# Kernel tuning notes

Measured on AMD Instinct MI355X. Metric: run time of the kernel, lower is better.

Reference implementation:

```python
import jax, jax.numpy as jnp
import numpy as np

B, S, D = 4, 2048, 256
H, RANK, DFF = 8, 8, 1024
DK = D // H
EPS = 1e-5


def _linear(x, W, b):
    # torch nn.Linear: y = x @ W.T + b, W shape (out, in)
    return jnp.einsum('bsd,od->bso', x, W) + b


def _layer_norm(x, g, b):
    mu = jnp.mean(x, axis=-1, keepdims=True)
    var = jnp.var(x, axis=-1, keepdims=True)
    return (x - mu) * jax.lax.rsqrt(var + EPS) * g + b


def setup_inputs() -> dict:
    key = jax.random.key(0)
    ks = jax.random.split(key, 20)
    r = RANK * H
    s = lambda fan_in: 1.0 / np.sqrt(fan_in)
    inp = {
        'x': jax.random.normal(ks[0], (B, S, D), jnp.float32),
        'Wq_down': jax.random.uniform(ks[1], (r, D), jnp.float32, -s(D), s(D)),
        'bq_down': jnp.zeros((r,), jnp.float32),
        'Wq_up': jax.random.uniform(ks[2], (D, r), jnp.float32, -s(r), s(r)),
        'bq_up': jnp.zeros((D,), jnp.float32),
        'Wk_down': jax.random.uniform(ks[3], (r, D), jnp.float32, -s(D), s(D)),
        'bk_down': jnp.zeros((r,), jnp.float32),
        'Wk_up': jax.random.uniform(ks[4], (D, r), jnp.float32, -s(r), s(r)),
        'bk_up': jnp.zeros((D,), jnp.float32),
        'Wv': jax.random.uniform(ks[5], (D, D), jnp.float32, -s(D), s(D)),
        'bv': jnp.zeros((D,), jnp.float32),
        'Wo': jax.random.uniform(ks[6], (D, D), jnp.float32, -s(D), s(D)),
        'bo': jnp.zeros((D,), jnp.float32),
        'ln_attn_g': jnp.ones((D,), jnp.float32),
        'ln_attn_b': jnp.zeros((D,), jnp.float32),
        'W_ff1': jax.random.uniform(ks[7], (DFF, D), jnp.float32, -s(D), s(D)),
        'b_ff1': jnp.zeros((DFF,), jnp.float32),
        'W_ff2': jax.random.uniform(ks[8], (D, DFF), jnp.float32, -s(DFF), s(DFF)),
        'b_ff2': jnp.zeros((D,), jnp.float32),
        'ln_blk_g': jnp.ones((D,), jnp.float32),
        'ln_blk_b': jnp.zeros((D,), jnp.float32),
    }
    return inp


def reference(x, Wq_down, bq_down, Wq_up, bq_up, Wk_down, bk_down, Wk_up, bk_up,
              Wv, bv, Wo, bo, ln_attn_g, ln_attn_b,
              W_ff1, b_ff1, W_ff2, b_ff2, ln_blk_g, ln_blk_b):
    # Low-rank Q/K: down-project to rank*H then up-project to D
    Q = _linear(_linear(x, Wq_down, bq_down), Wq_up, bq_up)
    K = _linear(_linear(x, Wk_down, bk_down), Wk_up, bk_up)
    V = _linear(x, Wv, bv)
    # (B,S,D) -> (B,H,S,DK)
    Q = Q.reshape(B, S, H, DK).transpose(0, 2, 1, 3)
    K = K.reshape(B, S, H, DK).transpose(0, 2, 1, 3)
    V = V.reshape(B, S, H, DK).transpose(0, 2, 1, 3)
    scale = 1.0 / np.sqrt(DK).astype(np.float32)
    scores = jnp.einsum('bhqd,bhkd->bhqk', Q, K) * scale
    attn = jax.nn.softmax(scores, axis=-1)
    context = jnp.einsum('bhqk,bhkd->bhqd', attn, V)
    context = context.transpose(0, 2, 1, 3).reshape(B, S, D)
    attn_out = _linear(context, Wo, bo)
    attn_out = _layer_norm(x + attn_out, ln_attn_g, ln_attn_b)
    # FFN: Linear -> GELU (exact erf, torch default) -> Linear
    h = jax.nn.gelu(_linear(attn_out, W_ff1, b_ff1), approximate=False)
    ff = _linear(h, W_ff2, b_ff2)
    return _layer_norm(attn_out + ff, ln_blk_g, ln_blk_b)
```

## Files before the change

### kernel.cpp

```cpp
#include <hip/hip_runtime.h>
#include <hip/hip_bf16.h>
#include <math.h>

#define NB 4
#define NS 2048
#define ND 256
#define NH 8
#define NDK 32
#define NDFF 1024
#define NROWS (NB * NS)
#define KC 2
#define KVB 64
#define KTILES (NS / KC / KVB)

using short8 = __attribute__((ext_vector_type(8))) short;
using f32x4  = __attribute__((ext_vector_type(4))) float;

__device__ __forceinline__ unsigned short f2bf(float f) {
  union { float f; unsigned u; } v; v.f = f;
  unsigned r = v.u + 0x7fffu + ((v.u >> 16) & 1u);
  return (unsigned short)(r >> 16);
}
__device__ __forceinline__ float bf2f(unsigned short u) {
  union { unsigned u; float f; } v; v.u = ((unsigned)u) << 16;
  return v.f;
}
__device__ __forceinline__ unsigned cvt_pk_bf16(float lo, float hi) {
  unsigned r;
  asm("v_cvt_pk_bf16_f32 %0, %1, %2" : "=v"(r) : "v"(lo), "v"(hi));
  return r;
}
__device__ __forceinline__ void gl_lds16(const void* g, void* l) {
  __builtin_amdgcn_global_load_lds(
      (const __attribute__((address_space(1))) unsigned int*)g,
      (__attribute__((address_space(3))) unsigned int*)l, 16, 0, 0);
}

__global__ void cvt_batch(const float* s0, const float* s1, const float* s2,
                          const float* s3, const float* s4, const float* s5,
                          const float* s6, const float* s7, const float* s8,
                          unsigned short* d0, unsigned short* d1,
                          unsigned short* d2, unsigned short* d3,
                          unsigned short* d4, unsigned short* d5,
                          unsigned short* d6, unsigned short* d7,
                          unsigned short* d8,
                          int n0, int n1, int n2, int n3, int n4, int n5,
                          int n6, int n7, int n8) {
  const float* s; unsigned short* d; int n;
  switch (blockIdx.y) {
    case 0: s = s0; d = d0; n = n0; break;
    case 1: s = s1; d = d1; n = n1; break;
    case 2: s = s2; d = d2; n = n2; break;
    case 3: s = s3; d = d3; n = n3; break;
    case 4: s = s4; d = d4; n = n4; break;
    case 5: s = s5; d = d5; n = n5; break;
    case 6: s = s6; d = d6; n = n6; break;
    case 7: s = s7; d = d7; n = n7; break;
    default: s = s8; d = d8; n = n8; break;
  }
  for (int i = (blockIdx.x * 256 + threadIdx.x) * 4; i < n; i += 512 * 256 * 4) {
    float4 v = *reinterpret_cast<const float4*>(s + i);
    ushort4 o;
    o.x = f2bf(v.x); o.y = f2bf(v.y); o.z = f2bf(v.z); o.w = f2bf(v.w);
    *reinterpret_cast<ushort4*>(d + i) = o;
  }
}

template <int BM, int ACT, int OBF, int RES>
__global__ __launch_bounds__(256)
void gemm_nt(const unsigned short* __restrict__ A, int lda,
             const unsigned short* __restrict__ W,
             const float* __restrict__ bias, const float* __restrict__ bias2,
             int bsplit, const float* __restrict__ resid,
             void* __restrict__ outp, int K, int O) {
  constexpr int MFW = BM / 32;
  __shared__ __align__(16) unsigned short lA[2][BM * 64];
  __shared__ __align__(16) unsigned short lB[2][64 * 64];
  const int tid = threadIdx.x, lane = tid & 63, wid = tid >> 6;
  const int wr = wid >> 1, wc = wid & 1;
  const int l15 = lane & 15, lg = lane >> 4;
  const int bm = blockIdx.x, bn = blockIdx.y;

  auto stage = [&](int k0, int buf) {
#pragma unroll
    for (int it = 0; it < BM / 32; ++it) {
      int c = it * 256 + tid;
      int row = c >> 3, cc = (c & 7) ^ (row & 7);
      gl_lds16(A + (size_t)(bm * BM + row) * lda + k0 + cc * 8,
               &lA[buf][c * 8]);
    }
#pragma unroll
    for (int it = 0; it < 2; ++it) {
      int c = it * 256 + tid;
      int row = c >> 3, cc = (c & 7) ^ (row & 7);
      gl_lds16(W + (size_t)(bn * 64 + row) * K + k0 + cc * 8, &lB[buf][c * 8]);
    }
  };

  f32x4 acc[MFW][2];
#pragma unroll
  for (int i = 0; i < MFW; ++i)
#pragma unroll
    for (int j = 0; j < 2; ++j) acc[i][j] = (f32x4)0.0f;

  const int T = K >> 6;
  stage(0, 0);
  __syncthreads();
  for (int t = 0; t < T; ++t) {
    const int cur = t & 1;
    if (t + 1 < T) stage((t + 1) << 6, cur ^ 1);
#pragma unroll
    for (int kk = 0; kk < 2; ++kk) {
      short8 a[MFW], b[2];
#pragma unroll
      for (int mf = 0; mf < MFW; ++mf) {
        int row = wr * (BM / 2) + mf * 16 + l15;
        a[mf] = *reinterpret_cast<const short8*>(
            &lA[cur][row * 64 + (((kk * 4 + lg) ^ (l15 & 7)) << 3)]);
      }
#pragma unroll
      for (int nf = 0; nf < 2; ++nf) {
        int row = wc * 32 + nf * 16 + l15;
        b[nf] = *reinterpret_cast<const short8*>(
            &lB[cur][row * 64 + (((kk * 4 + lg) ^ (l15 & 7)) << 3)]);
      }
#pragma unroll
      for (int mf = 0; mf < MFW; ++mf)
#pragma unroll
        for (int nf = 0; nf < 2; ++nf)
          acc[mf][nf] = __builtin_amdgcn_mfma_f32_16x16x32_bf16(
              a[mf], b[nf], acc[mf][nf], 0, 0, 0);
    }
    __syncthreads();
  }

#pragma unroll
  for (int mf = 0; mf < MFW; ++mf)
#pragma unroll
    for (int nf = 0; nf < 2; ++nf) {
      int col = bn * 64 + wc * 32 + nf * 16 + l15;
      float bv = (bias2 && col >= bsplit) ? bias2[col - bsplit] : bias[col];
#pragma unroll
      for (int i = 0; i < 4; ++i) {
        int row = bm * BM + wr * (BM / 2) + mf * 16 + lg * 4 + i;
        float v = acc[mf][nf][i] + bv;
        if (ACT == 1) v = 0.5f * v * (1.0f + erff(v * 0.70710678118654752f));
        if (RES) v += resid[(size_t)row * O + col];
        if (OBF)
          ((unsigned short*)outp)[(size_t)row * O + col] = f2bf(v);
        else
          ((float*)outp)[(size_t)row * O + col] = v;
      }
    }
}

__global__ __launch_bounds__(256)
void attn_kernel(const unsigned short* __restrict__ Qb,
                 const unsigned short* __restrict__ Kb,
                 const unsigned short* __restrict__ Vb,
                 unsigned short* __restrict__ pacc,
                 float* __restrict__ pl) {
  __shared__ __align__(16) unsigned short lK[2][KVB * 32];
  __shared__ __align__(16) unsigned short lVt[2][32 * 72];
  __shared__ __align__(16) unsigned short lP[4][16 * 64];
  const int tid = threadIdx.x, lane = tid & 63, wid = tid >> 6;
  const int l15 = lane & 15, lg = lane >> 4;
  const int qt = blockIdx.x, bh = blockIdx.y, kc = blockIdx.z;
  const int b = bh >> 3, h = bh & 7;
  const size_t headoff = (size_t)h * NDK;
  const int qbase = qt * 128 + wid * 32;
  const int kv0 = kc * (NS / KC);
  const float qscale = 0.25508686f;

  short8 aq[2];
#pragma unroll
  for (int r = 0; r < 2; ++r) {
    short8 v = *reinterpret_cast<const short8*>(
        Qb + (size_t)(b * NS + qbase + r * 16 + l15) * ND + headoff + lg * 8);
#pragma unroll
    for (int j = 0; j < 8; ++j)
      v[j] = (short)f2bf(bf2f((unsigned short)v[j]) * qscale);
    aq[r] = v;
  }

  const unsigned short* kptr =
      Kb + (size_t)(b * NS + kv0 + (tid >> 2)) * ND + headoff + (tid & 3) * 8;
  const int vd0 = (tid & 15) * 2, vk0 = (tid >> 4) * 4;
  const unsigned short* vptr =
      Vb + (size_t)(b * NS + kv0 + vk0) * ND + headoff + vd0;
  const size_t kvstride = (size_t)KVB * ND;

  auto writeV = [&](const unsigned* w, int buf) {
    unsigned lo0 = (w[0] & 0xffffu) | (w[1] << 16);
    unsigned lo1 = (w[2] & 0xffffu) | (w[3] << 16);
    unsigned hi0 = (w[0] >> 16) | (w[1] & 0xffff0000u);
    unsigned hi1 = (w[2] >> 16) | (w[3] & 0xffff0000u);
    *reinterpret_cast<uint2*>(&lVt[buf][vd0 * 72 + vk0]) = make_uint2(lo0, lo1);
    *reinterpret_cast<uint2*>(&lVt[buf][(vd0 + 1) * 72 + vk0]) =
        make_uint2(hi0, hi1);
  };

  f32x4 accT[2][2];
#pragma unroll
  for (int r = 0; r < 2; ++r)
#pragma unroll
    for (int d = 0; d < 2; ++d) accT[r][d] = (f32x4)0.0f;
  float l[2] = {0.0f, 0.0f};

  unsigned vr[4];
  gl_lds16(kptr, &lK[0][tid * 8]);
#pragma unroll
  for (int u = 0; u < 4; ++u)
    vr[u] = *reinterpret_cast<const unsigned*>(vptr + (size_t)u * ND);
  writeV(vr, 0);
  __syncthreads();

  for (int kt = 0; kt < KTILES; ++kt) {
    const int cur = kt & 1, nxt = cur ^ 1;
    const bool pf = (kt + 1 < KTILES);
    if (pf) {
      kptr += kvstride;
      vptr += kvstride;
      gl_lds16(kptr, &lK[nxt][tid * 8]);
#pragma unroll
      for (int u = 0; u < 4; ++u)
        vr[u] = *reinterpret_cast<const unsigned*>(vptr + (size_t)u * ND);
    }

#pragma unroll
    for (int r = 0; r < 2; ++r) {
      f32x4 sT[4];
      __builtin_amdgcn_s_setprio(1);
#pragma unroll
      for (int t = 0; t < 4; ++t) {
        short8 bk = *reinterpret_cast<const short8*>(
            &lK[cur][(t * 16 + l15) * 32 + lg * 8]);
        sT[t] = __builtin_amdgcn_mfma_f32_16x16x32_bf16(
            bk, aq[r], (f32x4)0.0f, 0, 0, 0);
      }
      __builtin_amdgcn_s_setprio(0);
#pragma unroll
      for (int t = 0; t < 4; ++t) {
        float p0 = __builtin_amdgcn_exp2f(sT[t][0]);
        float p1 = __builtin_amdgcn_exp2f(sT[t][1]);
        float p2 = __builtin_amdgcn_exp2f(sT[t][2]);
        float p3 = __builtin_amdgcn_exp2f(sT[t][3]);
        l[r] += (p0 + p1) + (p2 + p3);
        unsigned w0 = cvt_pk_bf16(p0, p1);
        unsigned w1 = cvt_pk_bf16(p2, p3);
        int blk = (t << 1) | (lg >> 1);
        *reinterpret_cast<uint2*>(
            &lP[wid][l15 * 64 + ((blk ^ (l15 & 7)) << 3) + ((lg & 1) << 2)]) =
            make_uint2(w0, w1);
      }
      __builtin_amdgcn_s_setprio(1);
#pragma unroll
      for (int kk = 0; kk < 2; ++kk) {
        short8 pa = *reinterpret_cast<const short8*>(
            &lP[wid][l15 * 64 + (((kk * 4 + lg) ^ (l15 & 7)) << 3)]);
#pragma unroll
        for (int dt = 0; dt < 2; ++dt) {
          short8 bv = *reinterpret_cast<const short8*>(
              &lVt[cur][(dt * 16 + l15) * 72 + kk * 32 + lg * 8]);
          accT[r][dt] = __builtin_amdgcn_mfma_f32_16x16x32_bf16(
              bv, pa, accT[r][dt], 0, 0, 0);
        }
      }
      __builtin_amdgcn_s_setprio(0);
    }

    if (pf) writeV(vr, nxt);
    __syncthreads();
  }

#pragma unroll
  for (int r = 0; r < 2; ++r) {
    l[r] += __shfl_xor(l[r], 16);
    l[r] += __shfl_xor(l[r], 32);
  }

#pragma unroll
  for (int r = 0; r < 2; ++r) {
    int qg = qbase + r * 16 + l15;
    size_t rowbase = ((size_t)kc * 65536 + (size_t)bh * NS + qg) * 32;
#pragma unroll
    for (int dt = 0; dt < 2; ++dt) {
      unsigned w0 = cvt_pk_bf16(accT[r][dt][0], accT[r][dt][1]);
      unsigned w1 = cvt_pk_bf16(accT[r][dt][2], accT[r][dt][3]);
      *reinterpret_cast<uint2*>(&pacc[rowbase + dt * 16 + lg * 4]) =
          make_uint2(w0, w1);
    }
  }
  if (lane < 16) {
#pragma unroll
    for (int r = 0; r < 2; ++r) {
      int qg = qbase + r * 16 + l15;
      pl[(size_t)kc * 65536 + (size_t)bh * NS + qg] = l[r];
    }
  }
}

__global__ __launch_bounds__(256)
void attn_combine(const unsigned short* __restrict__ pacc,
                  const float* __restrict__ pl,
                  unsigned short* __restrict__ ctx) {
  int gid = blockIdx.x * 256 + threadIdx.x;
  int r = gid >> 2, d8 = (gid & 3) * 8;
  float L = 0.0f;
#pragma unroll
  for (int c = 0; c < KC; ++c) L += pl[(size_t)c * 65536 + r];
  float inv = 1.0f / L;
  float o[8];
#pragma unroll
  for (int j = 0; j < 8; ++j) o[j] = 0.0f;
#pragma unroll
  for (int c = 0; c < KC; ++c) {
    short8 a = *reinterpret_cast<const short8*>(
        &pacc[((size_t)c * 65536 + r) * 32 + d8]);
#pragma unroll
    for (int j = 0; j < 8; ++j) o[j] += bf2f((unsigned short)a[j]);
  }
  int bh = r >> 11, q = r & 2047;
  int b = bh >> 3, h = bh & 7;
  short8 out;
#pragma unroll
  for (int j = 0; j < 8; ++j) out[j] = (short)f2bf(o[j] * inv);
  *reinterpret_cast<short8*>(
      &ctx[((size_t)(b * NS + q)) * ND + h * 32 + d8]) = out;
}

__global__ __launch_bounds__(256)
void ln_res_kernel(const float* __restrict__ a, const float* bsrc,
                   const float* __restrict__ g, const float* __restrict__ be,
                   float* yf, unsigned short* yb) {
  int row = blockIdx.x * 4 + (threadIdx.x >> 6);
  int lane = threadIdx.x & 63;
  size_t off = (size_t)row * ND + lane * 4;
  float4 va = *reinterpret_cast<const float4*>(a + off);
  float v0 = va.x, v1 = va.y, v2 = va.z, v3 = va.w;
  if (bsrc) {
    float4 vb = *reinterpret_cast<const float4*>(bsrc + off);
    v0 += vb.x; v1 += vb.y; v2 += vb.z; v3 += vb.w;
  }
  float s = v0 + v1 + v2 + v3;
  float sq = v0 * v0 + v1 * v1 + v2 * v2 + v3 * v3;
#pragma unroll
  for (int o = 1; o < 64; o <<= 1) {
    s += __shfl_xor(s, o);
    sq += __shfl_xor(sq, o);
  }
  float mu = s * (1.0f / 256.0f);
  float var = sq * (1.0f / 256.0f) - mu * mu;
  float rs = rsqrtf(var + 1e-5f);
  float4 vg = *reinterpret_cast<const float4*>(g + lane * 4);
  float4 vbe = *reinterpret_cast<const float4*>(be + lane * 4);
  float o0 = (v0 - mu) * rs * vg.x + vbe.x;
  float o1 = (v1 - mu) * rs * vg.y + vbe.y;
  float o2 = (v2 - mu) * rs * vg.z + vbe.z;
  float o3 = (v3 - mu) * rs * vg.w + vbe.w;
  if (yf) *reinterpret_cast<float4*>(yf + off) = make_float4(o0, o1, o2, o3);
  if (yb) {
    ushort4 ob;
    ob.x = f2bf(o0); ob.y = f2bf(o1); ob.z = f2bf(o2); ob.w = f2bf(o3);
    *reinterpret_cast<ushort4*>(yb + off) = ob;
  }
}

extern "C" void kernel_launch(void* const* d_in, const int* in_sizes, int n_in,
                              void* d_out, int out_size, void* d_ws,
                              size_t ws_size, hipStream_t stream) {
  (void)in_sizes; (void)n_in; (void)out_size; (void)ws_size;
  const float* x   = (const float*)d_in[0];
  const float* Wqd = (const float*)d_in[1];
  const float* bqd = (const float*)d_in[2];
  const float* Wqu = (const float*)d_in[3];
  const float* bqu = (const float*)d_in[4];
  const float* Wkd = (const float*)d_in[5];
  const float* bkd = (const float*)d_in[6];
  const float* Wku = (const float*)d_in[7];
  const float* bku = (const float*)d_in[8];
  const float* Wv  = (const float*)d_in[9];
  const float* bv  = (const float*)d_in[10];
  const float* Wo  = (const float*)d_in[11];
  const float* bo  = (const float*)d_in[12];
  const float* g1  = (const float*)d_in[13];
  const float* be1 = (const float*)d_in[14];
  const float* Wf1 = (const float*)d_in[15];
  const float* bf1 = (const float*)d_in[16];
  const float* Wf2 = (const float*)d_in[17];
  const float* bf2 = (const float*)d_in[18];
  const float* g2  = (const float*)d_in[19];
  const float* be2 = (const float*)d_in[20];

  char* p = (char*)d_ws;
  auto alloc = [&](size_t bytes) {
    char* r = p;
    p += (bytes + 255) & ~(size_t)255;
    return r;
  };
  unsigned short* xb   = (unsigned short*)alloc((size_t)NROWS * ND * 2);
  unsigned short* wqkd = (unsigned short*)alloc(128 * 256 * 2);
  unsigned short* wqu  = (unsigned short*)alloc(256 * 64 * 2);
  unsigned short* wku  = (unsigned short*)alloc(256 * 64 * 2);
  unsigned short* wv   = (unsigned short*)alloc(256 * 256 * 2);
  unsigned short* wo   = (unsigned short*)alloc(256 * 256 * 2);
  unsigned short* wf1  = (unsigned short*)alloc(1024 * 256 * 2);
  unsigned short* wf2  = (unsigned short*)alloc(256 * 1024 * 2);
  unsigned short* qkd  = (unsigned short*)alloc((size_t)NROWS * 128 * 2);
  unsigned short* Qb   = (unsigned short*)alloc((size_t)NROWS * ND * 2);
  unsigned short* Kb   = (unsigned short*)alloc((size_t)NROWS * ND * 2);
  unsigned short* Vb   = (unsigned short*)alloc((size_t)NROWS * ND * 2);
  unsigned short* ctx  = (unsigned short*)alloc((size_t)NROWS * ND * 2);
  float*          y1   = (float*)alloc((size_t)NROWS * ND * 4);
  unsigned short* y1b  = (unsigned short*)alloc((size_t)NROWS * ND * 2);
  unsigned short* hb   = (unsigned short*)alloc((size_t)NROWS * NDFF * 2);
  float* ao = (float*)d_out;

  unsigned short* pacc = hb;
  float* pl = y1;

  cvt_batch<<<dim3(512, 9), 256, 0, stream>>>(
      x, Wqd, Wkd, Wqu, Wku, Wv, Wo, Wf1, Wf2,
      xb, wqkd, wqkd + 64 * 256, wqu, wku, wv, wo, wf1, wf2,
      NROWS * ND, 64 * 256, 64 * 256, 256 * 64, 256 * 64, 256 * 256,
      256 * 256, 1024 * 256, 256 * 1024);

  gemm_nt<64, 0, 1, 0><<<dim3(128, 2), 256, 0, stream>>>(
      xb, 256, wqkd, bqd, bkd, 64, nullptr, qkd, 256, 128);
  gemm_nt<64, 0, 1, 0><<<dim3(128, 4), 256, 0, stream>>>(
      qkd, 128, wqu, bqu, nullptr, 0, nullptr, Qb, 64, 256);
  gemm_nt<64, 0, 1, 0><<<dim3(128, 4), 256, 0, stream>>>(
      qkd + 64, 128, wku, bku, nullptr, 0, nullptr, Kb, 64, 256);
  gemm_nt<64, 0, 1, 0><<<dim3(128, 4), 256, 0, stream>>>(
      xb, 256, wv, bv, nullptr, 0, nullptr, Vb, 256, 256);

  attn_kernel<<<dim3(NS / 128, NB * NH, KC), 256, 0, stream>>>(
      Qb, Kb, Vb, pacc, pl);
  attn_combine<<<dim3(1024), 256, 0, stream>>>(pacc, pl, ctx);

  gemm_nt<64, 0, 0, 1><<<dim3(128, 4), 256, 0, stream>>>(
      ctx, 256, wo, bo, nullptr, 0, x, ao, 256, 256);
  ln_res_kernel<<<NROWS / 4, 256, 0, stream>>>(ao, nullptr, g1, be1, y1, y1b);

  gemm_nt<128, 1, 1, 0><<<dim3(64, 16), 256, 0, stream>>>(
      y1b, 256, wf1, bf1, nullptr, 0, nullptr, hb, 256, NDFF);
  gemm_nt<64, 0, 0, 1><<<dim3(128, 4), 256, 0, stream>>>(
      hb, 1024, wf2, bf2, nullptr, 0, y1, ao, 1024, 256);
  ln_res_kernel<<<NROWS / 4, 256, 0, stream>>>(ao, nullptr, g2, be2,
                                               (float*)d_out, nullptr);
}
```

Before: 116.0 us.

## Fuse V projection into QK-down GEMM and batch Q/K up-projections into one launch

```diff
diff --git a/kernel.cpp b/kernel.cpp
--- a/kernel.cpp
+++ b/kernel.cpp
@@ -12,6 +12,7 @@
 #define KC 2
 #define KVB 64
 #define KTILES (NS / KC / KVB)
+#define QVLD 384
 
 using short8 = __attribute__((ext_vector_type(8))) short;
 using f32x4  = __attribute__((ext_vector_type(4))) float;
@@ -66,13 +67,16 @@
   }
 }
 
-template <int BM, int ACT, int OBF, int RES>
+template <int BM, int ACT, int OBF, int RES, int DUAL>
 __global__ __launch_bounds__(256)
 void gemm_nt(const unsigned short* __restrict__ A, int lda,
              const unsigned short* __restrict__ W,
              const float* __restrict__ bias, const float* __restrict__ bias2,
-             int bsplit, const float* __restrict__ resid,
-             void* __restrict__ outp, int K, int O) {
+             int bsplit, const float* __restrict__ bias3, int bsplit2,
+             const float* __restrict__ resid, void* __restrict__ outp,
+             int K, int O,
+             const unsigned short* A2, const unsigned short* W2,
+             const float* biasB, void* outp2) {
   constexpr int MFW = BM / 32;
   __shared__ __align__(16) unsigned short lA[2][BM * 64];
   __shared__ __align__(16) unsigned short lB[2][64 * 64];
@@ -81,19 +85,25 @@
   const int l15 = lane & 15, lg = lane >> 4;
   const int bm = blockIdx.x, bn = blockIdx.y;
 
+  const unsigned short* Ap = A;
+  const unsigned short* Wp = W;
+  const float* biasp = bias;
+  void* outpp = outp;
+  if (DUAL && blockIdx.z) { Ap = A2; Wp = W2; biasp = biasB; outpp = outp2; }
+
   auto stage = [&](int k0, int buf) {
 #pragma unroll
     for (int it = 0; it < BM / 32; ++it) {
       int c = it * 256 + tid;
       int row = c >> 3, cc = (c & 7) ^ (row & 7);
-      gl_lds16(A + (size_t)(bm * BM + row) * lda + k0 + cc * 8,
+      gl_lds16(Ap + (size_t)(bm * BM + row) * lda + k0 + cc * 8,
                &lA[buf][c * 8]);
     }
 #pragma unroll
     for (int it = 0; it < 2; ++it) {
       int c = it * 256 + tid;
       int row = c >> 3, cc = (c & 7) ^ (row & 7);
-      gl_lds16(W + (size_t)(bn * 64 + row) * K + k0 + cc * 8, &lB[buf][c * 8]);
+      gl_lds16(Wp + (size_t)(bn * 64 + row) * K + k0 + cc * 8, &lB[buf][c * 8]);
     }
   };
 
@@ -139,7 +149,10 @@
 #pragma unroll
     for (int nf = 0; nf < 2; ++nf) {
       int col = bn * 64 + wc * 32 + nf * 16 + l15;
-      float bv = (bias2 && col >= bsplit) ? bias2[col - bsplit] : bias[col];
+      float bv;
+      if (bias3 && col >= bsplit2) bv = bias3[col - bsplit2];
+      else if (bias2 && col >= bsplit) bv = bias2[col - bsplit];
+      else bv = biasp[col];
 #pragma unroll
       for (int i = 0; i < 4; ++i) {
         int row = bm * BM + wr * (BM / 2) + mf * 16 + lg * 4 + i;
@@ -147,9 +160,9 @@
         if (ACT == 1) v = 0.5f * v * (1.0f + erff(v * 0.70710678118654752f));
         if (RES) v += resid[(size_t)row * O + col];
         if (OBF)
-          ((unsigned short*)outp)[(size_t)row * O + col] = f2bf(v);
+          ((unsigned short*)outpp)[(size_t)row * O + col] = f2bf(v);
         else
-          ((float*)outp)[(size_t)row * O + col] = v;
+          ((float*)outpp)[(size_t)row * O + col] = v;
       }
     }
 }
@@ -157,7 +170,7 @@
 __global__ __launch_bounds__(256)
 void attn_kernel(const unsigned short* __restrict__ Qb,
                  const unsigned short* __restrict__ Kb,
-                 const unsigned short* __restrict__ Vb,
+                 const unsigned short* __restrict__ qv,
                  unsigned short* __restrict__ pacc,
                  float* __restrict__ pl) {
   __shared__ __align__(16) unsigned short lK[2][KVB * 32];
@@ -165,7 +178,7 @@
   __shared__ __align__(16) unsigned short lP[4][16 * 64];
   const int tid = threadIdx.x, lane = tid & 63, wid = tid >> 6;
   const int l15 = lane & 15, lg = lane >> 4;
-  const int qt = blockIdx.x, bh = blockIdx.y, kc = blockIdx.z;
+  const int bh = blockIdx.x, qt = blockIdx.y, kc = blockIdx.z;
   const int b = bh >> 3, h = bh & 7;
   const size_t headoff = (size_t)h * NDK;
   const int qbase = qt * 128 + wid * 32;
@@ -187,8 +200,7 @@
       Kb + (size_t)(b * NS + kv0 + (tid >> 2)) * ND + headoff + (tid & 3) * 8;
   const int vd0 = (tid & 15) * 2, vk0 = (tid >> 4) * 4;
   const unsigned short* vptr =
-      Vb + (size_t)(b * NS + kv0 + vk0) * ND + headoff + vd0;
-  const size_t kvstride = (size_t)KVB * ND;
+      qv + (size_t)(b * NS + kv0 + vk0) * QVLD + 128 + headoff + vd0;
 
   auto writeV = [&](const unsigned* w, int buf) {
     unsigned lo0 = (w[0] & 0xffffu) | (w[1] << 16);
@@ -211,7 +223,7 @@
   gl_lds16(kptr, &lK[0][tid * 8]);
 #pragma unroll
   for (int u = 0; u < 4; ++u)
-    vr[u] = *reinterpret_cast<const unsigned*>(vptr + (size_t)u * ND);
+    vr[u] = *reinterpret_cast<const unsigned*>(vptr + (size_t)u * QVLD);
   writeV(vr, 0);
   __syncthreads();
 
@@ -219,12 +231,12 @@
     const int cur = kt & 1, nxt = cur ^ 1;
     const bool pf = (kt + 1 < KTILES);
     if (pf) {
-      kptr += kvstride;
-      vptr += kvstride;
+      kptr += (size_t)KVB * ND;
+      vptr += (size_t)KVB * QVLD;
       gl_lds16(kptr, &lK[nxt][tid * 8]);
 #pragma unroll
       for (int u = 0; u < 4; ++u)
-        vr[u] = *reinterpret_cast<const unsigned*>(vptr + (size_t)u * ND);
+        vr[u] = *reinterpret_cast<const unsigned*>(vptr + (size_t)u * QVLD);
     }
 
 #pragma unroll
@@ -330,7 +342,7 @@
 }
 
 __global__ __launch_bounds__(256)
-void ln_res_kernel(const float* __restrict__ a, const float* bsrc,
+void ln_res_kernel(const float* __restrict__ a,
                    const float* __restrict__ g, const float* __restrict__ be,
                    float* yf, unsigned short* yb) {
   int row = blockIdx.x * 4 + (threadIdx.x >> 6);
@@ -338,10 +350,6 @@
   size_t off = (size_t)row * ND + lane * 4;
   float4 va = *reinterpret_cast<const float4*>(a + off);
   float v0 = va.x, v1 = va.y, v2 = va.z, v3 = va.w;
-  if (bsrc) {
-    float4 vb = *reinterpret_cast<const float4*>(bsrc + off);
-    v0 += vb.x; v1 += vb.y; v2 += vb.z; v3 += vb.w;
-  }
   float s = v0 + v1 + v2 + v3;
   float sq = v0 * v0 + v1 * v1 + v2 * v2 + v3 * v3;
 #pragma unroll
@@ -399,17 +407,15 @@
     return r;
   };
   unsigned short* xb   = (unsigned short*)alloc((size_t)NROWS * ND * 2);
-  unsigned short* wqkd = (unsigned short*)alloc(128 * 256 * 2);
+  unsigned short* wqkv = (unsigned short*)alloc(384 * 256 * 2);
   unsigned short* wqu  = (unsigned short*)alloc(256 * 64 * 2);
   unsigned short* wku  = (unsigned short*)alloc(256 * 64 * 2);
-  unsigned short* wv   = (unsigned short*)alloc(256 * 256 * 2);
   unsigned short* wo   = (unsigned short*)alloc(256 * 256 * 2);
   unsigned short* wf1  = (unsigned short*)alloc(1024 * 256 * 2);
   unsigned short* wf2  = (unsigned short*)alloc(256 * 1024 * 2);
-  unsigned short* qkd  = (unsigned short*)alloc((size_t)NROWS * 128 * 2);
+  unsigned short* qv   = (unsigned short*)alloc((size_t)NROWS * QVLD * 2);
   unsigned short* Qb   = (unsigned short*)alloc((size_t)NROWS * ND * 2);
   unsigned short* Kb   = (unsigned short*)alloc((size_t)NROWS * ND * 2);
-  unsigned short* Vb   = (unsigned short*)alloc((size_t)NROWS * ND * 2);
   unsigned short* ctx  = (unsigned short*)alloc((size_t)NROWS * ND * 2);
   float*          y1   = (float*)alloc((size_t)NROWS * ND * 4);
   unsigned short* y1b  = (unsigned short*)alloc((size_t)NROWS * ND * 2);
@@ -421,31 +427,32 @@
 
   cvt_batch<<<dim3(512, 9), 256, 0, stream>>>(
       x, Wqd, Wkd, Wqu, Wku, Wv, Wo, Wf1, Wf2,
-      xb, wqkd, wqkd + 64 * 256, wqu, wku, wv, wo, wf1, wf2,
+      xb, wqkv, wqkv + 64 * 256, wqu, wku, wqkv + 128 * 256, wo, wf1, wf2,
       NROWS * ND, 64 * 256, 64 * 256, 256 * 64, 256 * 64, 256 * 256,
       256 * 256, 1024 * 256, 256 * 1024);
 
-  gemm_nt<64, 0, 1, 0><<<dim3(128, 2), 256, 0, stream>>>(
-      xb, 256, wqkd, bqd, bkd, 64, nullptr, qkd, 256, 128);
-  gemm_nt<64, 0, 1, 0><<<dim3(128, 4), 256, 0, stream>>>(
-      qkd, 128, wqu, bqu, nullptr, 0, nullptr, Qb, 64, 256);
-  gemm_nt<64, 0, 1, 0><<<dim3(128, 4), 256, 0, stream>>>(
-      qkd + 64, 128, wku, bku, nullptr, 0, nullptr, Kb, 64, 256);
-  gemm_nt<64, 0, 1, 0><<<dim3(128, 4), 256, 0, stream>>>(
-      xb, 256, wv, bv, nullptr, 0, nullptr, Vb, 256, 256);
-
-  attn_kernel<<<dim3(NS / 128, NB * NH, KC), 256, 0, stream>>>(
-      Qb, Kb, Vb, pacc, pl);
+  gemm_nt<64, 0, 1, 0, 0><<<dim3(128, 6), 256, 0, stream>>>(
+      xb, 256, wqkv, bqd, bkd, 64, bv, 128, nullptr, qv, 256, QVLD,
+      nullptr, nullptr, nullptr, nullptr);
+  gemm_nt<64, 0, 1, 0, 1><<<dim3(128, 4, 2), 256, 0, stream>>>(
+      qv, QVLD, wqu, bqu, nullptr, 0, nullptr, 0, nullptr, Qb, 64, 256,
+      qv + 64, wku, bku, Kb);
+
+  attn_kernel<<<dim3(NB * NH, NS / 128, KC), 256, 0, stream>>>(
+      Qb, Kb, qv, pacc, pl);
   attn_combine<<<dim3(1024), 256, 0, stream>>>(pacc, pl, ctx);
 
-  gemm_nt<64, 0, 0, 1><<<dim3(128, 4), 256, 0, stream>>>(
-      ctx, 256, wo, bo, nullptr, 0, x, ao, 256, 256);
-  ln_res_kernel<<<NROWS / 4, 256, 0, stream>>>(ao, nullptr, g1, be1, y1, y1b);
-
-  gemm_nt<128, 1, 1, 0><<<dim3(64, 16), 256, 0, stream>>>(
-      y1b, 256, wf1, bf1, nullptr, 0, nullptr, hb, 256, NDFF);
-  gemm_nt<64, 0, 0, 1><<<dim3(128, 4), 256, 0, stream>>>(
-      hb, 1024, wf2, bf2, nullptr, 0, y1, ao, 1024, 256);
-  ln_res_kernel<<<NROWS / 4, 256, 0, stream>>>(ao, nullptr, g2, be2,
+  gemm_nt<64, 0, 0, 1, 0><<<dim3(128, 4), 256, 0, stream>>>(
+      ctx, 256, wo, bo, nullptr, 0, nullptr, 0, x, ao, 256, 256,
+      nullptr, nullptr, nullptr, nullptr);
+  ln_res_kernel<<<NROWS / 4, 256, 0, stream>>>(ao, g1, be1, y1, y1b);
+
+  gemm_nt<128, 1, 1, 0, 0><<<dim3(64, 16), 256, 0, stream>>>(
+      y1b, 256, wf1, bf1, nullptr, 0, nullptr, 0, nullptr, hb, 256, NDFF,
+      nullptr, nullptr, nullptr, nullptr);
+  gemm_nt<64, 0, 0, 1, 0><<<dim3(128, 4), 256, 0, stream>>>(
+      hb, 1024, wf2, bf2, nullptr, 0, nullptr, 0, y1, ao, 1024, 256,
+      nullptr, nullptr, nullptr, nullptr);
+  ln_res_kernel<<<NROWS / 4, 256, 0, stream>>>(ao, g2, be2,
                                                (float*)d_out, nullptr);
 }
```

New measurement: 113.1 us. 1.03x faster.
